# Kernel optimization log

Measured on AMD Instinct MI355X. Metric: run time of the kernel, lower is better.

Reference implementation:

```python
import jax, jax.numpy as jnp
import numpy as np
from functools import partial

N_LAYER = 6
D_MODEL = 512
D_INNER = 2 * D_MODEL  # expand=2
D_CONV = 4
EPS = 1e-5


def layer_norm(x, w, b, eps=EPS):
    mu = jnp.mean(x, axis=-1, keepdims=True)
    var = jnp.var(x, axis=-1, keepdims=True)
    return (x - mu) * jax.lax.rsqrt(var + eps) * w + b


def causal_dwconv1d(x, w, b):
    # x: (B, T, Di), w: (Di, d_conv), b: (Di,)
    # torch Conv1d(groups=Di, padding=d_conv-1) then [:, :, :T] == left-pad causal conv
    xc = jnp.transpose(x, (0, 2, 1))  # (B, Di, T)
    k = w[:, None, :]  # (Di, 1, d_conv)
    y = jax.lax.conv_general_dilated(
        xc, k, window_strides=(1,), padding=[(D_CONV - 1, 0)],
        dimension_numbers=("NCH", "OIH", "NCH"), feature_group_count=D_INNER)
    y = y + b[None, :, None]
    return jnp.transpose(y, (0, 2, 1))  # (B, T, Di)


def gru(x, wih, whh, bih, bhh):
    # x: (B, T, Di); PyTorch GRU math, h0 = 0
    B, T, Di = x.shape
    x_ih = jnp.einsum('btd,gd->btg', x, wih) + bih  # (B, T, 3Di)
    x_ih = jnp.transpose(x_ih, (1, 0, 2))  # (T, B, 3Di)
    whh_T = whh.T  # (Di, 3Di)

    def step(h, xg):
        hg = h @ whh_T + bhh  # (B, 3Di)
        xr, xz, xn = jnp.split(xg, 3, axis=-1)
        hr, hz, hn = jnp.split(hg, 3, axis=-1)
        r = jax.nn.sigmoid(xr + hr)
        z = jax.nn.sigmoid(xz + hz)
        n = jnp.tanh(xn + r * hn)
        h_new = (1.0 - z) * n + z * h
        return h_new, h_new

    h0 = jnp.zeros((B, Di), dtype=x.dtype)
    _, hs = jax.lax.scan(step, h0, x_ih)
    return jnp.transpose(hs, (1, 0, 2))  # (B, T, Di)


def mamba_fallback(x, in_w, in_b, conv_w, conv_b, wih, whh, bih, bhh, out_w, out_b):
    xz = jnp.einsum('btd,ed->bte', x, in_w) + in_b  # (B, T, 2Di)
    x_proj, z = jnp.split(xz, 2, axis=-1)
    x_conv = jax.nn.silu(causal_dwconv1d(x_proj, conv_w, conv_b))
    x_out = gru(x_conv, wih, whh, bih, bhh)
    x_out = x_out * jax.nn.silu(z)
    return jnp.einsum('bte,de->btd', x_out, out_w) + out_b


def setup_inputs() -> dict:
    key = jax.random.key(0)
    ks = jax.random.split(key, 16)
    L, D, Di = N_LAYER, D_MODEL, D_INNER
    s = 0.02
    inp = {
        "x": jax.random.normal(ks[0], (4, 1024, D), dtype=jnp.float32),
        "norm_w": jnp.ones((L, D), jnp.float32),
        "norm_b": jnp.zeros((L, D), jnp.float32),
        "in_proj_w": jax.random.normal(ks[1], (L, 2 * Di, D), jnp.float32) * s,
        "in_proj_b": jnp.zeros((L, 2 * Di), jnp.float32),
        "conv_w": jax.random.normal(ks[2], (L, Di, D_CONV), jnp.float32) * 0.2,
        "conv_b": jnp.zeros((L, Di), jnp.float32),
        "gru_wih": jax.random.normal(ks[3], (L, 3 * Di, Di), jnp.float32) * s,
        "gru_whh": jax.random.normal(ks[4], (L, 3 * Di, Di), jnp.float32) * s,
        "gru_bih": jnp.zeros((L, 3 * Di), jnp.float32),
        "gru_bhh": jnp.zeros((L, 3 * Di), jnp.float32),
        "out_w": jax.random.normal(ks[5], (L, D, Di), jnp.float32) * s,
        "out_b": jnp.zeros((L, D), jnp.float32),
        "normf_w": jnp.ones((D,), jnp.float32),
        "normf_b": jnp.zeros((D,), jnp.float32),
    }
    return inp


def reference(x, norm_w, norm_b, in_proj_w, in_proj_b, conv_w, conv_b,
              gru_wih, gru_whh, gru_bih, gru_bhh, out_w, out_b, normf_w, normf_b):
    hidden = x
    residual = None
    for i in range(N_LAYER):
        residual = hidden + residual if residual is not None else hidden
        hidden = layer_norm(residual, norm_w[i], norm_b[i])
        hidden = mamba_fallback(hidden, in_proj_w[i], in_proj_b[i], conv_w[i], conv_b[i],
                                gru_wih[i], gru_whh[i], gru_bih[i], gru_bhh[i],
                                out_w[i], out_b[i])
    residual = hidden + residual
    return layer_norm(residual, normf_w, normf_b)
```

## Files before the change

### kernel.cpp

```cpp
#include <hip/hip_runtime.h>
#include <hip/hip_bf16.h>
#include <stdint.h>

#define SEQ   1024
#define NB    4
#define BT    4096
#define DM    512
#define DI    1024
#define NL    6
#define CHUNK 64
#define NCH   16
#define NSLOT (NL + NCH - 1)

typedef float  f32x4  __attribute__((ext_vector_type(4)));
typedef short  bf16x8 __attribute__((ext_vector_type(8)));
typedef _Float16 f16x2 __attribute__((ext_vector_type(2)));
typedef uint32_t u32x4 __attribute__((ext_vector_type(4)));

__device__ __forceinline__ float bf2f(unsigned short u){
  union { unsigned int i; float f; } v; v.i = ((unsigned int)u) << 16; return v.f;
}
__device__ __forceinline__ unsigned short f2bf(float f){
  union { float f; unsigned int i; } v; v.f = f;
  unsigned int x = v.i;
  return (unsigned short)((x + 0x7fffu + ((x >> 16) & 1u)) >> 16);
}
__device__ __forceinline__ float bits2f(uint32_t u){
  union { uint32_t i; float f; } v; v.i = u; return v.f;
}
__device__ __forceinline__ f16x2 u2h(uint32_t u){
  union { uint32_t u; f16x2 h; } v; v.u = u; return v.h;
}
__device__ __forceinline__ float h16lo(uint32_t u){
  union { uint32_t u; f16x2 h; } v; v.u = u; return (float)v.h.x;
}
__device__ __forceinline__ uint32_t pkrtz2u(float a, float b){
  union { __fp16 __attribute__((ext_vector_type(2))) h; uint32_t u; } v;
  v.h = __builtin_amdgcn_cvt_pkrtz(a, b);
  return v.u;
}
__device__ __forceinline__ uint32_t packf16(float a, float b){
  union { _Float16 h[2]; uint32_t u; } v;
  v.h[0] = (_Float16)a; v.h[1] = (_Float16)b; return v.u;
}
__device__ __forceinline__ float sigmoidf_(float x){ return __fdividef(1.f, 1.f + __expf(-x)); }
__device__ __forceinline__ float siluf_(float x){ return x * __fdividef(1.f, 1.f + __expf(-x)); }
__device__ __forceinline__ float tanhf_(float x){
  float e = __expf(2.f*x);
  return 1.f - __fdividef(2.f, e + 1.f);
}

__global__ __launch_bounds__(256) void cvtwt_kernel(const float* __restrict__ whh,
                                                    uint32_t* __restrict__ wT){
  const int n = NL*64*96*256;
  for (int idx = blockIdx.x*256 + threadIdx.x; idx < n; idx += gridDim.x*256){
    int tid = idx & 255;
    int rest = idx >> 8;
    int j = rest % 96;
    int rest2 = rest / 96;
    int g = rest2 & 63;
    int l = rest2 >> 6;
    int il = tid >> 4, ks = tid & 15;
    int i = g*16 + il;
    int G = j >> 5, jj = j & 31;
    int k = ks*64 + 2*jj;
    const float* src = whh + ((size_t)l*3072 + G*1024 + i)*1024 + k;
    wT[idx] = packf16(src[0], src[1]);
  }
}

__global__ __launch_bounds__(256) void lnres_slot(
    int slot, const float* __restrict__ x,
    const float* __restrict__ norm_w, const float* __restrict__ norm_b,
    float* __restrict__ hidden_ring,
    float* __restrict__ resid_ring,
    float* __restrict__ resid5,
    unsigned short* __restrict__ lnbf)
{
  const int l = blockIdx.z, c = slot - l;
  if (c < 0 || c >= NCH) return;
  const int wave = threadIdx.x >> 6;
  const int lane = threadIdx.x & 63;
  const int r = blockIdx.x*4 + wave;
  const int b = r >> 6, dt = r & 63;
  const int tg = c*CHUNK + dt;
  const int p = c & 1;

  const float* hid = (l == 0) ? x + ((size_t)b*SEQ + tg)*DM + lane*8
                              : hidden_ring + (((size_t)(l-1)*2 + p)*256 + r)*DM + lane*8;
  float4 a0 = *(const float4*)hid;
  float4 a1 = *(const float4*)(hid + 4);
  if (l > 0){
    const float* rin = resid_ring + (((size_t)(l-1)*2 + p)*256 + r)*DM + lane*8;
    float4 b0 = *(const float4*)rin;
    float4 b1 = *(const float4*)(rin + 4);
    a0.x+=b0.x; a0.y+=b0.y; a0.z+=b0.z; a0.w+=b0.w;
    a1.x+=b1.x; a1.y+=b1.y; a1.z+=b1.z; a1.w+=b1.w;
  }
  float* rout = (l == 5) ? resid5 + ((size_t)b*SEQ + tg)*DM + lane*8
                         : resid_ring + (((size_t)l*2 + p)*256 + r)*DM + lane*8;
  *(float4*)rout = a0;
  *(float4*)(rout + 4) = a1;

  float xv[8] = {a0.x,a0.y,a0.z,a0.w,a1.x,a1.y,a1.z,a1.w};
  float s = 0.f, sq = 0.f;
  #pragma unroll
  for (int q=0;q<8;q++){ s += xv[q]; sq += xv[q]*xv[q]; }
  #pragma unroll
  for (int off=32; off; off>>=1){ s += __shfl_xor(s, off); sq += __shfl_xor(sq, off); }
  float mean = s * (1.f/DM);
  float var  = sq * (1.f/DM) - mean*mean;
  float rstd = rsqrtf(var + 1e-5f);
  const float* gamma = norm_w + l*DM;
  const float* beta  = norm_b + l*DM;
  float4 g0 = *(const float4*)(gamma + lane*8);
  float4 g1 = *(const float4*)(gamma + lane*8 + 4);
  float4 e0 = *(const float4*)(beta  + lane*8);
  float4 e1 = *(const float4*)(beta  + lane*8 + 4);
  float gv[8] = {g0.x,g0.y,g0.z,g0.w,g1.x,g1.y,g1.z,g1.w};
  float ev[8] = {e0.x,e0.y,e0.z,e0.w,e1.x,e1.y,e1.z,e1.w};
  uint4 pk;
  float y0 = (xv[0]-mean)*rstd*gv[0]+ev[0], y1 = (xv[1]-mean)*rstd*gv[1]+ev[1];
  float y2 = (xv[2]-mean)*rstd*gv[2]+ev[2], y3 = (xv[3]-mean)*rstd*gv[3]+ev[3];
  float y4 = (xv[4]-mean)*rstd*gv[4]+ev[4], y5 = (xv[5]-mean)*rstd*gv[5]+ev[5];
  float y6 = (xv[6]-mean)*rstd*gv[6]+ev[6], y7 = (xv[7]-mean)*rstd*gv[7]+ev[7];
  pk.x = (unsigned)f2bf(y0) | ((unsigned)f2bf(y1)<<16);
  pk.y = (unsigned)f2bf(y2) | ((unsigned)f2bf(y3)<<16);
  pk.z = (unsigned)f2bf(y4) | ((unsigned)f2bf(y5)<<16);
  pk.w = (unsigned)f2bf(y6) | ((unsigned)f2bf(y7)<<16);
  *(uint4*)(lnbf + ((size_t)l*256 + r)*DM + lane*8) = pk;
}

__global__ __launch_bounds__(256) void ln_final(
    const float* __restrict__ hidden, const float* __restrict__ resid_in,
    const float* __restrict__ gamma,  const float* __restrict__ beta,
    float* __restrict__ out_f32)
{
  int wave = threadIdx.x >> 6;
  int lane = threadIdx.x & 63;
  int row  = blockIdx.x*4 + wave;
  size_t base = (size_t)row * DM + lane*8;
  float4 a0 = *(const float4*)(hidden + base);
  float4 a1 = *(const float4*)(hidden + base + 4);
  float4 b0 = *(const float4*)(resid_in + base);
  float4 b1 = *(const float4*)(resid_in + base + 4);
  a0.x+=b0.x; a0.y+=b0.y; a0.z+=b0.z; a0.w+=b0.w;
  a1.x+=b1.x; a1.y+=b1.y; a1.z+=b1.z; a1.w+=b1.w;
  float xv[8] = {a0.x,a0.y,a0.z,a0.w,a1.x,a1.y,a1.z,a1.w};
  float s = 0.f, sq = 0.f;
  #pragma unroll
  for (int q=0;q<8;q++){ s += xv[q]; sq += xv[q]*xv[q]; }
  #pragma unroll
  for (int off=32; off; off>>=1){ s += __shfl_xor(s, off); sq += __shfl_xor(sq, off); }
  float mean = s * (1.f/DM);
  float var  = sq * (1.f/DM) - mean*mean;
  float rstd = rsqrtf(var + 1e-5f);
  float4 g0 = *(const float4*)(gamma + lane*8);
  float4 g1 = *(const float4*)(gamma + lane*8 + 4);
  float4 e0 = *(const float4*)(beta  + lane*8);
  float4 e1 = *(const float4*)(beta  + lane*8 + 4);
  float gv[8] = {g0.x,g0.y,g0.z,g0.w,g1.x,g1.y,g1.z,g1.w};
  float ev[8] = {e0.x,e0.y,e0.z,e0.w,e1.x,e1.y,e1.z,e1.w};
  float4 o0, o1;
  o0.x=(xv[0]-mean)*rstd*gv[0]+ev[0]; o0.y=(xv[1]-mean)*rstd*gv[1]+ev[1];
  o0.z=(xv[2]-mean)*rstd*gv[2]+ev[2]; o0.w=(xv[3]-mean)*rstd*gv[3]+ev[3];
  o1.x=(xv[4]-mean)*rstd*gv[4]+ev[4]; o1.y=(xv[5]-mean)*rstd*gv[5]+ev[5];
  o1.z=(xv[6]-mean)*rstd*gv[6]+ev[6]; o1.w=(xv[7]-mean)*rstd*gv[7]+ev[7];
  *(float4*)(out_f32 + base)     = o0;
  *(float4*)(out_f32 + base + 4) = o1;
}

__device__ __forceinline__ bf16x8 ldcvt8(const float* p){
  float4 u = *(const float4*)p;
  float4 v = *(const float4*)(p + 4);
  bf16x8 r;
  r[0]=(short)f2bf(u.x); r[1]=(short)f2bf(u.y); r[2]=(short)f2bf(u.z); r[3]=(short)f2bf(u.w);
  r[4]=(short)f2bf(v.x); r[5]=(short)f2bf(v.y); r[6]=(short)f2bf(v.z); r[7]=(short)f2bf(v.w);
  return r;
}
__global__ __launch_bounds__(256) void gemm_slot(
    int op, int slot,
    const unsigned short* __restrict__ lnbf, const float* __restrict__ inw,
    const float* __restrict__ inb, float* __restrict__ xz_ring,
    const unsigned short* __restrict__ xconvb, const float* __restrict__ wih,
    const float* __restrict__ bih, unsigned short* __restrict__ xihb,
    const unsigned short* __restrict__ xoutb, const float* __restrict__ outw,
    const float* __restrict__ outb, float* __restrict__ hidden_ring,
    float* __restrict__ hidden5)
{
  const int l = blockIdx.z, c = slot - l;
  if (c < 0 || c >= NCH) return;

  const unsigned short* A; const float* Bf; const float* bias;
  int N, K;
  if (op == 0){ A = lnbf   + (size_t)l*256*DM;  Bf = inw  + (size_t)l*2048*512;  bias = inb  + l*2048; N = 2048; K = 512; }
  else if (op == 1){ A = xconvb + (size_t)l*256*DI; Bf = wih  + (size_t)l*3072*1024; bias = bih  + l*3072; N = 3072; K = 1024; }
  else { A = xoutb  + (size_t)l*256*DI; Bf = outw + (size_t)l*512*1024;  bias = outb + l*512;  N = 512;  K = 1024; }

  const int tid  = threadIdx.x;
  const int wid  = tid >> 6, lane = tid & 63;
  const int wm   = wid >> 1, wn = wid & 1;
  const int tm   = blockIdx.y*128 + wm*64;
  const int tn   = blockIdx.x*128 + wn*64;
  const int l15  = lane & 15;
  const int lk   = (lane >> 4) * 8;

  f32x4 acc[4][4] = {};
  for (int kk = 0; kk < K; kk += 32){
    bf16x8 a[4], b[4];
    #pragma unroll
    for (int f=0; f<4; ++f)
      a[f] = *(const bf16x8*)(A + (size_t)(tm + f*16 + l15)*K + kk + lk);
    #pragma unroll
    for (int f=0; f<4; ++f)
      b[f] = ldcvt8(Bf + (size_t)(tn + f*16 + l15)*K + kk + lk);
    #pragma unroll
    for (int i=0;i<4;i++)
      #pragma unroll
      for (int j=0;j<4;j++)
        acc[i][j] = __builtin_amdgcn_mfma_f32_16x16x32_bf16(a[i], b[j], acc[i][j], 0,0,0);
  }
  const int crow0 = (lane>>4)*4;
  const int p = c & 1;
  #pragma unroll
  for (int i=0;i<4;i++){
    #pragma unroll
    for (int j=0;j<4;j++){
      int col = tn + j*16 + l15;
      float bv = bias[col];
      #pragma unroll
      for (int r=0;r<4;r++){
        int row = tm + i*16 + crow0 + r;
        float val = acc[i][j][r] + bv;
        if (op == 0){
          xz_ring[(((size_t)l*2 + p)*256 + row)*2048 + col] = val;
        } else if (op == 1){
          xihb[((size_t)l*256 + row)*3072 + col] = f2bf(val);
        } else {
          if (l == 5){
            int b_ = row >> 6, dt = row & 63;
            hidden5[((size_t)b_*SEQ + c*CHUNK + dt)*DM + col] = val;
          } else {
            hidden_ring[(((size_t)l*2 + p)*256 + row)*DM + col] = val;
          }
        }
      }
    }
  }
}

__global__ __launch_bounds__(256) void conv_slot(
    int slot, const float* __restrict__ xz_ring,
    const float* __restrict__ cw, const float* __restrict__ cb,
    unsigned short* __restrict__ xconvb)
{
  const int l = blockIdx.z, c = slot - l;
  if (c < 0 || c >= NCH) return;
  const int idx = blockIdx.x*256 + threadIdx.x;
  const int ch = idx & (DI-1);
  const int r  = idx >> 10;
  const int b  = r >> 6, dt = r & 63;
  const int tg = c*CHUNK + dt;
  const int p  = c & 1;

  const float* base = xz_ring + ((size_t)l*2)*256*2048;
  float w0 = cw[(l*DI + ch)*4+0], w1 = cw[(l*DI + ch)*4+1];
  float w2 = cw[(l*DI + ch)*4+2], w3 = cw[(l*DI + ch)*4+3];
  float acc = cb[l*DI + ch] + base[((size_t)p*256 + r)*2048 + ch] * w3;
  #pragma unroll
  for (int k=1;k<=3;k++){
    float w = (k==1) ? w2 : (k==2) ? w1 : w0;
    if (tg >= k){
      int dtk = dt - k;
      int pp = (dtk >= 0) ? p : (p^1);
      int rr = b*64 + ((dtk + 64) & 63);
      acc += base[((size_t)pp*256 + rr)*2048 + ch] * w;
    }
  }
  xconvb[((size_t)l*256 + r)*DI + ch] = f2bf(siluf_(acc));
}

__global__ __launch_bounds__(256, 2) void scan_slot(
    int slot,
    const unsigned short* __restrict__ xihb,
    const float* __restrict__ xz_ring,
    const uint32_t* __restrict__ wT,
    const float* __restrict__ bhh,
    uint32_t* __restrict__ hbufs,
    unsigned short* __restrict__ xoutb)
{
  const int w = blockIdx.x;
  const int l = w >> 6;
  const int g = w & 63;
  const int c = slot - l;
  if (c < 0 || c >= NCH) return;

  const int tid = threadIdx.x;
  const int il  = tid >> 4;
  const int ks  = tid & 15;
  const int i   = g*16 + il;

  const uint32_t* pw = wT + ((size_t)(l*64 + g)*96)*256 + tid;
  uint32_t wrp[32], wzp[32], wnp[32];
  #pragma unroll
  for (int j=0;j<32;j++) wrp[j] = pw[(size_t)j*256];
  #pragma unroll
  for (int j=0;j<32;j++) wzp[j] = pw[(size_t)(32+j)*256];
  #pragma unroll
  for (int j=0;j<32;j++) wnp[j] = pw[(size_t)(64+j)*256];

  const float* bh = bhh + l*3072;
  const float bhr = bh[i], bhz = bh[DI+i], bhn = bh[2*DI+i];

  __shared__ uint32_t hshw[2][NB][16*36];

  const uint32_t lbase = (uint32_t)l << 10;
  uint32_t* hb = hbufs + (size_t)l*2*4096;
  const unsigned short* xih = xihb + (size_t)l*256*3072;
  const float* xzp = xz_ring + ((size_t)(l*2 + (c&1))*256)*2048;
  unsigned short* xo = xoutb + (size_t)l*256*DI;

  float xr_c[NB], xzg_c[NB], xn_c[NB], zg_c[NB];
  float xr_n[NB], xzg_n[NB], xn_n[NB], zg_n[NB];
  float hprev[NB] = {0.f,0.f,0.f,0.f};
  if (ks == 0){
    #pragma unroll
    for (int b4=0;b4<NB;b4++){
      int r = b4*64;
      xr_c[b4]  = bf2f(xih[(size_t)r*3072 + i]);
      xzg_c[b4] = bf2f(xih[(size_t)r*3072 + DI + i]);
      xn_c[b4]  = bf2f(xih[(size_t)r*3072 + 2*DI + i]);
      zg_c[b4]  = xzp[(size_t)r*2048 + DI + i];
    }
  }

  const int r0 = tid >> 6;
  const int c0 = tid & 63;

  for (int dt=0; dt<CHUNK; ++dt){
    const int t   = c*CHUNK + dt;
    const int par = t & 1;
    if (t == 0){
      uint32_t* hz = &hshw[0][0][0];
      for (int j=tid; j<NB*16*36; j+=256) hz[j] = 0u;
    } else {
      const uint32_t want = lbase + (uint32_t)t;
      const uintptr_t p = (uintptr_t)(hb + (size_t)par*4096 + 4*tid);
      u32x4 A0, A1, A2, A3;
      asm volatile("global_load_dwordx4 %0, %4, off sc1\n\t"
                   "global_load_dwordx4 %1, %5, off sc1\n\t"
                   "global_load_dwordx4 %2, %6, off sc1\n\t"
                   "global_load_dwordx4 %3, %7, off sc1\n\t"
                   "s_waitcnt vmcnt(0)"
                   : "=&v"(A0), "=&v"(A1), "=&v"(A2), "=&v"(A3)
                   : "v"(p), "v"(p+4096), "v"(p+8192), "v"(p+12288));
      while (((A0[0]>>16)<want)|((A0[1]>>16)<want)|((A0[2]>>16)<want)|((A0[3]>>16)<want)|
             ((A1[0]>>16)<want)|((A1[1]>>16)<want)|((A1[2]>>16)<want)|((A1[3]>>16)<want)|
             ((A2[0]>>16)<want)|((A2[1]>>16)<want)|((A2[2]>>16)<want)|((A2[3]>>16)<want)|
             ((A3[0]>>16)<want)|((A3[1]>>16)<want)|((A3[2]>>16)<want)|((A3[3]>>16)<want)){
        __builtin_amdgcn_s_sleep(8);
        asm volatile("global_load_dwordx4 %0, %4, off sc1\n\t"
                     "global_load_dwordx4 %1, %5, off sc1\n\t"
                     "global_load_dwordx4 %2, %6, off sc1\n\t"
                     "global_load_dwordx4 %3, %7, off sc1\n\t"
                     "s_waitcnt vmcnt(0)"
                     : "=&v"(A0), "=&v"(A1), "=&v"(A2), "=&v"(A3)
                     : "v"(p), "v"(p+4096), "v"(p+8192), "v"(p+12288));
      }
      uint16_t* hp16 = (uint16_t*)&hshw[par][0][0];
      #pragma unroll
      for (int b4=0;b4<NB;b4++){
        hp16[b4*1152 + (r0+ 0)*72 + c0] = (uint16_t)A0[b4];
        hp16[b4*1152 + (r0+ 4)*72 + c0] = (uint16_t)A1[b4];
        hp16[b4*1152 + (r0+ 8)*72 + c0] = (uint16_t)A2[b4];
        hp16[b4*1152 + (r0+12)*72 + c0] = (uint16_t)A3[b4];
      }
    }
    __syncthreads();

    if (ks == 0 && dt == 0 && c > 0){
      const uint16_t* hp16 = (const uint16_t*)&hshw[par][0][0];
      #pragma unroll
      for (int b4=0;b4<NB;b4++){
        union { uint16_t u; _Float16 h; } hv;
        hv.u = hp16[b4*1152 + (i>>6)*72 + (i&63)];
        hprev[b4] = (float)hv.h;
      }
    }
    if (ks == 0 && dt+1 < CHUNK){
      #pragma unroll
      for (int b4=0;b4<NB;b4++){
        int r = b4*64 + dt + 1;
        xr_n[b4]  = bf2f(xih[(size_t)r*3072 + i]);
        xzg_n[b4] = bf2f(xih[(size_t)r*3072 + DI + i]);
        xn_n[b4]  = bf2f(xih[(size_t)r*3072 + 2*DI + i]);
        zg_n[b4]  = xzp[(size_t)r*2048 + DI + i];
      }
    }

    float ar[NB] = {0,0,0,0}, az[NB] = {0,0,0,0}, an[NB] = {0,0,0,0};
    #pragma unroll
    for (int q=0;q<8;q++){
      #pragma unroll
      for (int b4=0;b4<NB;b4++){
        u32x4 hv = *(const u32x4*)&hshw[par][b4][ks*36 + 4*q];
        ar[b4] = __builtin_amdgcn_fdot2(u2h(wrp[4*q+0]), u2h(hv[0]), ar[b4], false);
        az[b4] = __builtin_amdgcn_fdot2(u2h(wzp[4*q+0]), u2h(hv[0]), az[b4], false);
        an[b4] = __builtin_amdgcn_fdot2(u2h(wnp[4*q+0]), u2h(hv[0]), an[b4], false);
        ar[b4] = __builtin_amdgcn_fdot2(u2h(wrp[4*q+1]), u2h(hv[1]), ar[b4], false);
        az[b4] = __builtin_amdgcn_fdot2(u2h(wzp[4*q+1]), u2h(hv[1]), az[b4], false);
        an[b4] = __builtin_amdgcn_fdot2(u2h(wnp[4*q+1]), u2h(hv[1]), an[b4], false);
        ar[b4] = __builtin_amdgcn_fdot2(u2h(wrp[4*q+2]), u2h(hv[2]), ar[b4], false);
        az[b4] = __builtin_amdgcn_fdot2(u2h(wzp[4*q+2]), u2h(hv[2]), az[b4], false);
        an[b4] = __builtin_amdgcn_fdot2(u2h(wnp[4*q+2]), u2h(hv[2]), an[b4], false);
        ar[b4] = __builtin_amdgcn_fdot2(u2h(wrp[4*q+3]), u2h(hv[3]), ar[b4], false);
        az[b4] = __builtin_amdgcn_fdot2(u2h(wzp[4*q+3]), u2h(hv[3]), az[b4], false);
        an[b4] = __builtin_amdgcn_fdot2(u2h(wnp[4*q+3]), u2h(hv[3]), an[b4], false);
      }
    }
    #pragma unroll
    for (int off=1; off<16; off<<=1){
      #pragma unroll
      for (int b4=0;b4<NB;b4++){
        ar[b4] += __shfl_xor(ar[b4], off);
        az[b4] += __shfl_xor(az[b4], off);
        an[b4] += __shfl_xor(an[b4], off);
      }
    }

    if (ks == 0){
      u32x4 HW;
      const uint32_t ntag = (lbase + (uint32_t)t + 1u) << 16;
      #pragma unroll
      for (int b4=0;b4<NB;b4++){
        float r_ = sigmoidf_(xr_c[b4] + ar[b4] + bhr);
        float z_ = sigmoidf_(xzg_c[b4] + az[b4] + bhz);
        float n_ = tanhf_(xn_c[b4] + r_*(an[b4] + bhn));
        float hnew = (1.f - z_)*n_ + z_*hprev[b4];
        hprev[b4] = hnew;
        HW[b4] = (pkrtz2u(hnew, 0.f) & 0xffffu) | ntag;
        int r = b4*64 + dt;
        xo[(size_t)r*DI + i] = f2bf(hnew * siluf_(zg_c[b4]));
        xr_c[b4]=xr_n[b4]; xzg_c[b4]=xzg_n[b4]; xn_c[b4]=xn_n[b4]; zg_c[b4]=zg_n[b4];
      }
      const uintptr_t hdst = (uintptr_t)(hb + (size_t)((t+1)&1)*4096 + 4*i);
      asm volatile("global_store_dwordx4 %0, %1, off sc1"
                   :: "v"(hdst), "v"(HW));
    }
  }
}

extern "C" void kernel_launch(void* const* d_in, const int* in_sizes, int n_in,
                              void* d_out, int out_size, void* d_ws, size_t ws_size,
                              hipStream_t stream)
{
  (void)in_sizes; (void)n_in; (void)out_size; (void)ws_size;
  const float* x      = (const float*)d_in[0];
  const float* norm_w = (const float*)d_in[1];
  const float* norm_b = (const float*)d_in[2];
  const float* inw    = (const float*)d_in[3];
  const float* inb    = (const float*)d_in[4];
  const float* convw  = (const float*)d_in[5];
  const float* convb  = (const float*)d_in[6];
  const float* wih    = (const float*)d_in[7];
  const float* whh    = (const float*)d_in[8];
  const float* bih    = (const float*)d_in[9];
  const float* bhh    = (const float*)d_in[10];
  const float* outw   = (const float*)d_in[11];
  const float* outb   = (const float*)d_in[12];
  const float* normfw = (const float*)d_in[13];
  const float* normfb = (const float*)d_in[14];
  float* out = (float*)d_out;

  char* ws = (char*)d_ws;
  size_t off = 0;
  auto alloc = [&](size_t bytes)->void*{ void* p = ws + off; off = (off + bytes + 255) & ~(size_t)255; return p; };
  uint32_t*       wT      = (uint32_t*)      alloc((size_t)NL*64*96*256*4);
  unsigned short* lnbf    = (unsigned short*)alloc((size_t)NL*256*DM*2);
  float*          xz_ring = (float*)         alloc((size_t)NL*2*256*2048*4);
  unsigned short* xconvb  = (unsigned short*)alloc((size_t)NL*256*DI*2);
  unsigned short* xihb    = (unsigned short*)alloc((size_t)NL*256*3072*2);
  unsigned short* xoutb   = (unsigned short*)alloc((size_t)NL*256*DI*2);
  float*          resid_ring  = (float*)     alloc((size_t)NL*2*256*DM*4);
  float*          hidden_ring = (float*)     alloc((size_t)NL*2*256*DM*4);
  float*          resid5  = (float*)         alloc((size_t)BT*DM*4);
  float*          hidden5 = (float*)         alloc((size_t)BT*DM*4);
  uint32_t*       hbufs   = (uint32_t*)      alloc((size_t)NL*2*4096*4);

  hipMemsetAsync(hbufs, 0, (size_t)NL*2*4096*4, stream);
  cvtwt_kernel<<<2048, 256, 0, stream>>>(whh, wT);

  for (int slot = 0; slot < NSLOT; ++slot){
    lnres_slot<<<dim3(64,1,NL), 256, 0, stream>>>(slot, x, norm_w, norm_b,
                                                  hidden_ring, resid_ring, resid5, lnbf);
    gemm_slot<<<dim3(16,2,NL), 256, 0, stream>>>(0, slot, lnbf, inw, inb, xz_ring,
                                                 xconvb, wih, bih, xihb,
                                                 xoutb, outw, outb, hidden_ring, hidden5);
    conv_slot<<<dim3(1024,1,NL), 256, 0, stream>>>(slot, xz_ring, convw, convb, xconvb);
    gemm_slot<<<dim3(24,2,NL), 256, 0, stream>>>(1, slot, lnbf, inw, inb, xz_ring,
                                                 xconvb, wih, bih, xihb,
                                                 xoutb, outw, outb, hidden_ring, hidden5);
    scan_slot<<<dim3(NL*64), 256, 0, stream>>>(slot, xihb, xz_ring, wT, bhh, hbufs, xoutb);
    gemm_slot<<<dim3(4,2,NL), 256, 0, stream>>>(2, slot, lnbf, inw, inb, xz_ring,
                                                xconvb, wih, bih, xihb,
                                                xoutb, outw, outb, hidden_ring, hidden5);
  }
  ln_final<<<1024, 256, 0, stream>>>(hidden5, resid5, normfw, normfb, out);
}
```

Measured before the change: 11.77 ms.

## Split GRU recurrent dot products across 32 lanes per row with 512-thread blocks

Each hidden unit's recurrent matvec is now split over 32 lanes instead of 16, so each scan block uses 512 threads and each thread holds 48 packed fp16 weight registers instead of 96. The weight pre-pack kernel writes 16-byte vectors in the new layout, and the shared-memory h tile is reorganised to 32-column rows. This is meant to shorten the per-timestep dependent chain in the serial scan and lower register pressure. The cost is one more shuffle-reduction stage and more threads contending on the LDS and the spin-wait polling.

```diff
diff --git a/kernel.cpp b/kernel.cpp
--- a/kernel.cpp
+++ b/kernel.cpp
@@ -31,9 +31,6 @@
 __device__ __forceinline__ f16x2 u2h(uint32_t u){
   union { uint32_t u; f16x2 h; } v; v.u = u; return v.h;
 }
-__device__ __forceinline__ float h16lo(uint32_t u){
-  union { uint32_t u; f16x2 h; } v; v.u = u; return (float)v.h.x;
-}
 __device__ __forceinline__ uint32_t pkrtz2u(float a, float b){
   union { __fp16 __attribute__((ext_vector_type(2))) h; uint32_t u; } v;
   v.h = __builtin_amdgcn_cvt_pkrtz(a, b);
@@ -52,20 +49,26 @@
 
 __global__ __launch_bounds__(256) void cvtwt_kernel(const float* __restrict__ whh,
                                                     uint32_t* __restrict__ wT){
-  const int n = NL*64*96*256;
-  for (int idx = blockIdx.x*256 + threadIdx.x; idx < n; idx += gridDim.x*256){
-    int tid = idx & 255;
-    int rest = idx >> 8;
-    int j = rest % 96;
-    int rest2 = rest / 96;
+  const int n4 = NL*64*12*512;
+  u32x4* out4 = (u32x4*)wT;
+  for (int idx = blockIdx.x*256 + threadIdx.x; idx < n4; idx += gridDim.x*256){
+    int tid = idx & 511;
+    int rest = idx >> 9;
+    int j = rest % 12;
+    int rest2 = rest / 12;
     int g = rest2 & 63;
     int l = rest2 >> 6;
-    int il = tid >> 4, ks = tid & 15;
+    int il = tid >> 5, ks = tid & 31;
     int i = g*16 + il;
-    int G = j >> 5, jj = j & 31;
-    int k = ks*64 + 2*jj;
-    const float* src = whh + ((size_t)l*3072 + G*1024 + i)*1024 + k;
-    wT[idx] = packf16(src[0], src[1]);
+    int G = j >> 2, q = j & 3;
+    int kb = ks*32 + q*8;
+    const float* src = whh + ((size_t)l*3072 + G*1024 + i)*1024 + kb;
+    u32x4 v;
+    v[0] = packf16(src[0], src[1]);
+    v[1] = packf16(src[2], src[3]);
+    v[2] = packf16(src[4], src[5]);
+    v[3] = packf16(src[6], src[7]);
+    out4[idx] = v;
   }
 }
 
@@ -280,7 +283,7 @@
   xconvb[((size_t)l*256 + r)*DI + ch] = f2bf(siluf_(acc));
 }
 
-__global__ __launch_bounds__(256, 2) void scan_slot(
+__global__ __launch_bounds__(512, 4) void scan_slot(
     int slot,
     const unsigned short* __restrict__ xihb,
     const float* __restrict__ xz_ring,
@@ -296,23 +299,23 @@
   if (c < 0 || c >= NCH) return;
 
   const int tid = threadIdx.x;
-  const int il  = tid >> 4;
-  const int ks  = tid & 15;
+  const int il  = tid >> 5;
+  const int ks  = tid & 31;
   const int i   = g*16 + il;
 
-  const uint32_t* pw = wT + ((size_t)(l*64 + g)*96)*256 + tid;
-  uint32_t wrp[32], wzp[32], wnp[32];
-  #pragma unroll
-  for (int j=0;j<32;j++) wrp[j] = pw[(size_t)j*256];
-  #pragma unroll
-  for (int j=0;j<32;j++) wzp[j] = pw[(size_t)(32+j)*256];
-  #pragma unroll
-  for (int j=0;j<32;j++) wnp[j] = pw[(size_t)(64+j)*256];
+  const u32x4* pw = (const u32x4*)wT + ((size_t)(l*64 + g)*12)*512 + tid;
+  u32x4 wr4[4], wz4[4], wn4[4];
+  #pragma unroll
+  for (int q=0;q<4;q++) wr4[q] = pw[(size_t)q*512];
+  #pragma unroll
+  for (int q=0;q<4;q++) wz4[q] = pw[(size_t)(4+q)*512];
+  #pragma unroll
+  for (int q=0;q<4;q++) wn4[q] = pw[(size_t)(8+q)*512];
 
   const float* bh = bhh + l*3072;
   const float bhr = bh[i], bhz = bh[DI+i], bhn = bh[2*DI+i];
 
-  __shared__ uint32_t hshw[2][NB][16*36];
+  __shared__ uint32_t hsh[2][NB][576];
 
   const uint32_t lbase = (uint32_t)l << 10;
   uint32_t* hb = hbufs + (size_t)l*2*4096;
@@ -334,56 +337,48 @@
     }
   }
 
-  const int r0 = tid >> 6;
-  const int c0 = tid & 63;
+  const int row0 = tid >> 5;
+  const int col0 = tid & 31;
 
   for (int dt=0; dt<CHUNK; ++dt){
     const int t   = c*CHUNK + dt;
     const int par = t & 1;
     if (t == 0){
-      uint32_t* hz = &hshw[0][0][0];
-      for (int j=tid; j<NB*16*36; j+=256) hz[j] = 0u;
+      uint32_t* hz = &hsh[0][0][0];
+      for (int j=tid; j<NB*576; j+=512) hz[j] = 0u;
     } else {
       const uint32_t want = lbase + (uint32_t)t;
       const uintptr_t p = (uintptr_t)(hb + (size_t)par*4096 + 4*tid);
-      u32x4 A0, A1, A2, A3;
-      asm volatile("global_load_dwordx4 %0, %4, off sc1\n\t"
-                   "global_load_dwordx4 %1, %5, off sc1\n\t"
-                   "global_load_dwordx4 %2, %6, off sc1\n\t"
-                   "global_load_dwordx4 %3, %7, off sc1\n\t"
+      u32x4 A0, A1;
+      asm volatile("global_load_dwordx4 %0, %2, off sc1\n\t"
+                   "global_load_dwordx4 %1, %3, off sc1\n\t"
                    "s_waitcnt vmcnt(0)"
-                   : "=&v"(A0), "=&v"(A1), "=&v"(A2), "=&v"(A3)
-                   : "v"(p), "v"(p+4096), "v"(p+8192), "v"(p+12288));
+                   : "=&v"(A0), "=&v"(A1)
+                   : "v"(p), "v"(p + 8192));
       while (((A0[0]>>16)<want)|((A0[1]>>16)<want)|((A0[2]>>16)<want)|((A0[3]>>16)<want)|
-             ((A1[0]>>16)<want)|((A1[1]>>16)<want)|((A1[2]>>16)<want)|((A1[3]>>16)<want)|
-             ((A2[0]>>16)<want)|((A2[1]>>16)<want)|((A2[2]>>16)<want)|((A2[3]>>16)<want)|
-             ((A3[0]>>16)<want)|((A3[1]>>16)<want)|((A3[2]>>16)<want)|((A3[3]>>16)<want)){
+             ((A1[0]>>16)<want)|((A1[1]>>16)<want)|((A1[2]>>16)<want)|((A1[3]>>16)<want)){
         __builtin_amdgcn_s_sleep(8);
-        asm volatile("global_load_dwordx4 %0, %4, off sc1\n\t"
-                     "global_load_dwordx4 %1, %5, off sc1\n\t"
-                     "global_load_dwordx4 %2, %6, off sc1\n\t"
-                     "global_load_dwordx4 %3, %7, off sc1\n\t"
+        asm volatile("global_load_dwordx4 %0, %2, off sc1\n\t"
+                     "global_load_dwordx4 %1, %3, off sc1\n\t"
                      "s_waitcnt vmcnt(0)"
-                     : "=&v"(A0), "=&v"(A1), "=&v"(A2), "=&v"(A3)
-                     : "v"(p), "v"(p+4096), "v"(p+8192), "v"(p+12288));
-      }
-      uint16_t* hp16 = (uint16_t*)&hshw[par][0][0];
+                     : "=&v"(A0), "=&v"(A1)
+                     : "v"(p), "v"(p + 8192));
+      }
+      uint16_t* hp16 = (uint16_t*)&hsh[par][0][0];
       #pragma unroll
       for (int b4=0;b4<NB;b4++){
-        hp16[b4*1152 + (r0+ 0)*72 + c0] = (uint16_t)A0[b4];
-        hp16[b4*1152 + (r0+ 4)*72 + c0] = (uint16_t)A1[b4];
-        hp16[b4*1152 + (r0+ 8)*72 + c0] = (uint16_t)A2[b4];
-        hp16[b4*1152 + (r0+12)*72 + c0] = (uint16_t)A3[b4];
+        hp16[b4*1152 + row0*36 + col0]      = (uint16_t)A0[b4];
+        hp16[b4*1152 + (row0+16)*36 + col0] = (uint16_t)A1[b4];
       }
     }
     __syncthreads();
 
     if (ks == 0 && dt == 0 && c > 0){
-      const uint16_t* hp16 = (const uint16_t*)&hshw[par][0][0];
+      const uint16_t* hp16 = (const uint16_t*)&hsh[par][0][0];
       #pragma unroll
       for (int b4=0;b4<NB;b4++){
         union { uint16_t u; _Float16 h; } hv;
-        hv.u = hp16[b4*1152 + (i>>6)*72 + (i&63)];
+        hv.u = hp16[b4*1152 + (i>>5)*36 + (i&31)];
         hprev[b4] = (float)hv.h;
       }
     }
@@ -400,26 +395,26 @@
 
     float ar[NB] = {0,0,0,0}, az[NB] = {0,0,0,0}, an[NB] = {0,0,0,0};
     #pragma unroll
-    for (int q=0;q<8;q++){
+    for (int q=0;q<4;q++){
       #pragma unroll
       for (int b4=0;b4<NB;b4++){
-        u32x4 hv = *(const u32x4*)&hshw[par][b4][ks*36 + 4*q];
-        ar[b4] = __builtin_amdgcn_fdot2(u2h(wrp[4*q+0]), u2h(hv[0]), ar[b4], false);
-        az[b4] = __builtin_amdgcn_fdot2(u2h(wzp[4*q+0]), u2h(hv[0]), az[b4], false);
-        an[b4] = __builtin_amdgcn_fdot2(u2h(wnp[4*q+0]), u2h(hv[0]), an[b4], false);
-        ar[b4] = __builtin_amdgcn_fdot2(u2h(wrp[4*q+1]), u2h(hv[1]), ar[b4], false);
-        az[b4] = __builtin_amdgcn_fdot2(u2h(wzp[4*q+1]), u2h(hv[1]), az[b4], false);
-        an[b4] = __builtin_amdgcn_fdot2(u2h(wnp[4*q+1]), u2h(hv[1]), an[b4], false);
-        ar[b4] = __builtin_amdgcn_fdot2(u2h(wrp[4*q+2]), u2h(hv[2]), ar[b4], false);
-        az[b4] = __builtin_amdgcn_fdot2(u2h(wzp[4*q+2]), u2h(hv[2]), az[b4], false);
-        an[b4] = __builtin_amdgcn_fdot2(u2h(wnp[4*q+2]), u2h(hv[2]), an[b4], false);
-        ar[b4] = __builtin_amdgcn_fdot2(u2h(wrp[4*q+3]), u2h(hv[3]), ar[b4], false);
-        az[b4] = __builtin_amdgcn_fdot2(u2h(wzp[4*q+3]), u2h(hv[3]), az[b4], false);
-        an[b4] = __builtin_amdgcn_fdot2(u2h(wnp[4*q+3]), u2h(hv[3]), an[b4], false);
-      }
-    }
-    #pragma unroll
-    for (int off=1; off<16; off<<=1){
+        u32x4 hv = *(const u32x4*)&hsh[par][b4][ks*18 + 4*q];
+        ar[b4] = __builtin_amdgcn_fdot2(u2h(wr4[q][0]), u2h(hv[0]), ar[b4], false);
+        az[b4] = __builtin_amdgcn_fdot2(u2h(wz4[q][0]), u2h(hv[0]), az[b4], false);
+        an[b4] = __builtin_amdgcn_fdot2(u2h(wn4[q][0]), u2h(hv[0]), an[b4], false);
+        ar[b4] = __builtin_amdgcn_fdot2(u2h(wr4[q][1]), u2h(hv[1]), ar[b4], false);
+        az[b4] = __builtin_amdgcn_fdot2(u2h(wz4[q][1]), u2h(hv[1]), az[b4], false);
+        an[b4] = __builtin_amdgcn_fdot2(u2h(wn4[q][1]), u2h(hv[1]), an[b4], false);
+        ar[b4] = __builtin_amdgcn_fdot2(u2h(wr4[q][2]), u2h(hv[2]), ar[b4], false);
+        az[b4] = __builtin_amdgcn_fdot2(u2h(wz4[q][2]), u2h(hv[2]), az[b4], false);
+        an[b4] = __builtin_amdgcn_fdot2(u2h(wn4[q][2]), u2h(hv[2]), an[b4], false);
+        ar[b4] = __builtin_amdgcn_fdot2(u2h(wr4[q][3]), u2h(hv[3]), ar[b4], false);
+        az[b4] = __builtin_amdgcn_fdot2(u2h(wz4[q][3]), u2h(hv[3]), az[b4], false);
+        an[b4] = __builtin_amdgcn_fdot2(u2h(wn4[q][3]), u2h(hv[3]), an[b4], false);
+      }
+    }
+    #pragma unroll
+    for (int off=1; off<32; off<<=1){
       #pragma unroll
       for (int b4=0;b4<NB;b4++){
         ar[b4] += __shfl_xor(ar[b4], off);
@@ -475,7 +470,7 @@
   char* ws = (char*)d_ws;
   size_t off = 0;
   auto alloc = [&](size_t bytes)->void*{ void* p = ws + off; off = (off + bytes + 255) & ~(size_t)255; return p; };
-  uint32_t*       wT      = (uint32_t*)      alloc((size_t)NL*64*96*256*4);
+  uint32_t*       wT      = (uint32_t*)      alloc((size_t)NL*64*12*512*16);
   unsigned short* lnbf    = (unsigned short*)alloc((size_t)NL*256*DM*2);
   float*          xz_ring = (float*)         alloc((size_t)NL*2*256*2048*4);
   unsigned short* xconvb  = (unsigned short*)alloc((size_t)NL*256*DI*2);
@@ -500,7 +495,7 @@
     gemm_slot<<<dim3(24,2,NL), 256, 0, stream>>>(1, slot, lnbf, inw, inb, xz_ring,
                                                  xconvb, wih, bih, xihb,
                                                  xoutb, outw, outb, hidden_ring, hidden5);
-    scan_slot<<<dim3(NL*64), 256, 0, stream>>>(slot, xihb, xz_ring, wT, bhh, hbufs, xoutb);
+    scan_slot<<<dim3(NL*64), 512, 0, stream>>>(slot, xihb, xz_ring, wT, bhh, hbufs, xoutb);
     gemm_slot<<<dim3(4,2,NL), 256, 0, stream>>>(2, slot, lnbf, inw, inb, xz_ring,
                                                 xconvb, wih, bih, xihb,
                                                 xoutb, outw, outb, hidden_ring, hidden5);
```

Result: slower. 13.56 ms (+15.3%).
